# Performance work log

Hardware: AMD Instinct MI355X
Metric: run time of the kernel (lower is better)

The kernel has to match this reference:

```python
import jax, jax.numpy as jnp
import numpy as np

N_NODES = 100000
N_EDGES = 1600000
D_IN = 128
D_HID = 128
D_OUT = 40


def _linear_init(key, fan_in, fan_out):
    # torch nn.Linear default: U(-1/sqrt(fan_in), 1/sqrt(fan_in)) for W and b
    kw, kb = jax.random.split(key)
    bound = 1.0 / np.sqrt(fan_in)
    W = jax.random.uniform(kw, (fan_in, fan_out), jnp.float32, -bound, bound)
    b = jax.random.uniform(kb, (fan_out,), jnp.float32, -bound, bound)
    return W, b


def setup_inputs() -> dict:
    key = jax.random.key(0)
    ks = jax.random.split(key, 8)
    x = jax.random.normal(ks[0], (N_NODES, D_IN), jnp.float32)
    edges = jax.random.randint(ks[1], (2, N_EDGES), 0, N_NODES, jnp.int64)
    # layer 0: MLP(128 -> 128 -> 128)
    W1_0, b1_0 = _linear_init(ks[2], D_IN, D_HID)
    W2_0, b2_0 = _linear_init(ks[3], D_HID, D_HID)
    # layer 1: MLP(128 -> 128 -> 128)
    W1_1, b1_1 = _linear_init(ks[4], D_HID, D_HID)
    W2_1, b2_1 = _linear_init(ks[5], D_HID, D_HID)
    # layer 2: MLP(128 -> 128 -> 40)
    W1_2, b1_2 = _linear_init(ks[6], D_HID, D_HID)
    W2_2, b2_2 = _linear_init(ks[7], D_HID, D_OUT)
    eps = jnp.zeros(())  # GINConv train_eps=True initializes eps=0
    return {
        "x": x, "edges": edges,
        "W1_0": W1_0, "b1_0": b1_0, "W2_0": W2_0, "b2_0": b2_0, "eps_0": eps,
        "W1_1": W1_1, "b1_1": b1_1, "W2_1": W2_1, "b2_1": b2_1, "eps_1": eps,
        "W1_2": W1_2, "b1_2": b1_2, "W2_2": W2_2, "b2_2": b2_2, "eps_2": eps,
    }


def _gin_conv(x, src, dst, eps, W1, b1, W2, b2):
    # sum-aggregate neighbor features: out_i = MLP((1+eps)*x_i + sum_{j->i} x_j)
    aggr = jax.ops.segment_sum(x[src], dst, num_segments=x.shape[0])
    h = (1.0 + eps) * x + aggr
    h = jnp.maximum(h @ W1 + b1, 0.0)  # MLP layer 1 + ReLU
    return h @ W2 + b2                  # MLP layer 2


def reference(x, edges,
              W1_0, b1_0, W2_0, b2_0, eps_0,
              W1_1, b1_1, W2_1, b2_1, eps_1,
              W1_2, b1_2, W2_2, b2_2, eps_2):
    src, dst = edges[0], edges[1]
    # dropout is identity at inference (training=False)
    h = jax.nn.relu(_gin_conv(x, src, dst, eps_0, W1_0, b1_0, W2_0, b2_0))
    h = jax.nn.relu(_gin_conv(h, src, dst, eps_1, W1_1, b1_1, W2_1, b2_1))
    o = _gin_conv(h, src, dst, eps_2, W1_2, b1_2, W2_2, b2_2)
    return jax.nn.log_softmax(o, axis=1)
```

## Files before the change

### kernel.cpp

```cpp
#include <hip/hip_runtime.h>
#include <stdint.h>

typedef __attribute__((ext_vector_type(8))) short short8;
typedef __attribute__((ext_vector_type(4))) float float4v;

__device__ __forceinline__ float bf2f(unsigned short s) {
    union { unsigned int u; float f; } c; c.u = ((unsigned int)s) << 16; return c.f;
}
__device__ __forceinline__ unsigned short f2bf(float f) {
    union { float f; unsigned int u; } c; c.f = f;
    unsigned int x = c.u;
    unsigned int r = x + 0x7fffu + ((x >> 16) & 1u);
    return (unsigned short)(r >> 16);
}
__device__ __forceinline__ void unpack2(unsigned int u, float& lo, float& hi) {
    union { unsigned int uu; float ff; } a, b;
    a.uu = u << 16;
    b.uu = u & 0xffff0000u;
    lo = a.ff; hi = b.ff;
}

__global__ __launch_bounds__(256) void bs_count(const int* __restrict__ dst, int nE,
                                                int* __restrict__ bucketCnt) {
    __shared__ int c[512];
    int t = threadIdx.x;
    for (int i = t; i < 512; i += 256) c[i] = 0;
    __syncthreads();
    int base = blockIdx.x * 4096;
    for (int i = t; i < 4096; i += 256) {
        int e = base + i;
        if (e < nE) atomicAdd(&c[dst[e] >> 8], 1);
    }
    __syncthreads();
    for (int i = t; i < 512; i += 256)
        if (c[i]) atomicAdd(&bucketCnt[i], c[i]);
}

__global__ __launch_bounds__(512) void bs_scan(const int* __restrict__ bucketCnt,
                                               int* __restrict__ bucketBase,
                                               int* __restrict__ bucketCur,
                                               int* __restrict__ off, int M, int nE) {
    __shared__ int s[512];
    int t = threadIdx.x;
    int v = bucketCnt[t];
    s[t] = v;
    __syncthreads();
    for (int o = 1; o < 512; o <<= 1) {
        int x = (t >= o) ? s[t - o] : 0;
        __syncthreads();
        s[t] += x;
        __syncthreads();
    }
    bucketBase[t] = s[t] - v;
    bucketCur[t] = s[t] - v;
    if (t == 511) bucketBase[512] = s[511];
    if (t == 0) off[M] = nE;
}

__global__ __launch_bounds__(512) void bs_scatter(const int* __restrict__ src,
                                                  const int* __restrict__ dst, int nE,
                                                  int* __restrict__ bucketCur,
                                                  unsigned int* __restrict__ ebuf) {
    __shared__ int cnt[512];
    __shared__ int excl[512];
    __shared__ int chunk[512];
    __shared__ unsigned int buf[4096];
    __shared__ unsigned short bkt[4096];
    int t = threadIdx.x;
    cnt[t] = 0;
    __syncthreads();
    int base = blockIdx.x * 4096;
    int n = nE - base; if (n > 4096) n = 4096;
    unsigned int pk[8]; int bk[8]; int rk[8];
#pragma unroll
    for (int u = 0; u < 8; ++u) {
        int i = t + u * 512;
        if (i < n) {
            int e = base + i;
            int d = dst[e];
            int b = d >> 8;
            bk[u] = b;
            pk[u] = (unsigned int)src[e] | ((unsigned int)(d & 255) << 17);
            rk[u] = atomicAdd(&cnt[b], 1);
        } else bk[u] = -1;
    }
    __syncthreads();
    excl[t] = cnt[t];
    __syncthreads();
    for (int o = 1; o < 512; o <<= 1) {
        int x = (t >= o) ? excl[t - o] : 0;
        __syncthreads();
        excl[t] += x;
        __syncthreads();
    }
    int ex = excl[t] - cnt[t];
    __syncthreads();
    excl[t] = ex;
    if (cnt[t]) chunk[t] = atomicAdd(&bucketCur[t], cnt[t]);
    __syncthreads();
#pragma unroll
    for (int u = 0; u < 8; ++u) {
        if (bk[u] >= 0) {
            int lp = excl[bk[u]] + rk[u];
            buf[lp] = pk[u];
            bkt[lp] = (unsigned short)bk[u];
        }
    }
    __syncthreads();
    for (int i = t; i < n; i += 512) {
        int b = bkt[i];
        ebuf[chunk[b] + (i - excl[b])] = buf[i];
    }
}

__global__ __launch_bounds__(512) void bs_build(const unsigned int* __restrict__ ebuf,
                                                const int* __restrict__ bucketBase,
                                                int* __restrict__ off,
                                                int* __restrict__ esrc, int M) {
    __shared__ int cnt[256];
    __shared__ int excl[256];
    __shared__ int obuf[5120];
    int t = threadIdx.x, b = blockIdx.x;
    int base = bucketBase[b];
    int n = bucketBase[b + 1] - base;
    if (t < 256) cnt[t] = 0;
    __syncthreads();
    unsigned int pk[10]; int dl[10]; int rk[10];
#pragma unroll
    for (int u = 0; u < 10; ++u) {
        int i = t + u * 512;
        if (i < n) {
            unsigned int p = ebuf[base + i];
            pk[u] = p;
            int d = (p >> 17) & 255;
            dl[u] = d;
            rk[u] = atomicAdd(&cnt[d], 1);
        } else dl[u] = -1;
    }
    __syncthreads();
    if (t < 256) excl[t] = cnt[t];
    __syncthreads();
    for (int o = 1; o < 256; o <<= 1) {
        int x = (t < 256 && t >= o) ? excl[t - o] : 0;
        __syncthreads();
        if (t < 256) excl[t] += x;
        __syncthreads();
    }
    if (t < 256) {
        int ex = excl[t] - cnt[t];
        int node = b * 256 + t;
        if (node < M) off[node] = base + ex;
        excl[t] = ex;
    }
    __syncthreads();
#pragma unroll
    for (int u = 0; u < 10; ++u) {
        if (dl[u] >= 0) {
            int lp = excl[dl[u]] + rk[u];
            if (lp < 5120) obuf[lp] = (int)(pk[u] & 0x1FFFF);
        }
    }
    __syncthreads();
    for (int i = t; i < n; i += 512) esrc[base + i] = obuf[i];
}

struct WPack {
    const float* W[6];
    unsigned short* hi[6];
};

__global__ __launch_bounds__(256) void k_wprep_all(WPack p) {
    int b = blockIdx.x;
    int mat = b >> 6;
    int rel = b - mat * 64;
    int NPAD = (mat == 5) ? 48 : 128;
    int N = (mat == 5) ? 40 : 128;
    int idx = rel * 256 + threadIdx.x;
    if (idx >= NPAD * 128) return;
    int n = idx >> 7, k = idx & 127;
    float w = (n < N) ? p.W[mat][k * N + n] : 0.f;
    p.hi[mat][idx] = f2bf(w);
}

__global__ __launch_bounds__(256) void k_cast(const float4* __restrict__ in,
                                              uint2* __restrict__ out, int n4) {
    int i = blockIdx.x * 256 + threadIdx.x;
    if (i >= n4) return;
    float4 v = in[i];
    uint2 o;
    o.x = ((unsigned int)f2bf(v.y) << 16) | f2bf(v.x);
    o.y = ((unsigned int)f2bf(v.w) << 16) | f2bf(v.z);
    out[i] = o;
}

__global__ __launch_bounds__(256) void k_aggr(const uint2* __restrict__ Hin,
                                              const int* __restrict__ off,
                                              const int* __restrict__ esrc,
                                              const float* __restrict__ epsp,
                                              uint2* __restrict__ Ahi,
                                              uint2* __restrict__ Alo, int M) {
    int w = threadIdx.x >> 6, lane = threadIdx.x & 63;
    int li = lane & 31, half = lane >> 5;
    int node = blockIdx.x * 4 + w;
    if (node >= M) return;
    float ep = 1.0f + epsp[0];
    uint2 ow = Hin[node * 32 + li];
    float s0 = 0.f, s1 = 0.f, s2 = 0.f, s3 = 0.f;
    int i = off[node], e = off[node + 1];
    for (; i + 16 <= e; i += 16) {
        uint2 v[8];
#pragma unroll
        for (int j = 0; j < 8; ++j) v[j] = Hin[esrc[i + 2 * j + half] * 32 + li];
#pragma unroll
        for (int j = 0; j < 8; ++j) {
            float a, b, c, d;
            unpack2(v[j].x, a, b);
            unpack2(v[j].y, c, d);
            s0 += a; s1 += b; s2 += c; s3 += d;
        }
    }
    for (; i + 2 <= e; i += 2) {
        uint2 v = Hin[esrc[i + half] * 32 + li];
        float a, b, c, d;
        unpack2(v.x, a, b);
        unpack2(v.y, c, d);
        s0 += a; s1 += b; s2 += c; s3 += d;
    }
    if (i < e && half == 0) {
        uint2 v = Hin[esrc[i] * 32 + li];
        float a, b, c, d;
        unpack2(v.x, a, b);
        unpack2(v.y, c, d);
        s0 += a; s1 += b; s2 += c; s3 += d;
    }
    s0 += __shfl_xor(s0, 32);
    s1 += __shfl_xor(s1, 32);
    s2 += __shfl_xor(s2, 32);
    s3 += __shfl_xor(s3, 32);
    if (half == 0) {
        float o0, o1, o2, o3;
        unpack2(ow.x, o0, o1);
        unpack2(ow.y, o2, o3);
        float r0 = ep * o0 + s0, r1 = ep * o1 + s1;
        float r2 = ep * o2 + s2, r3 = ep * o3 + s3;
        unsigned short h0 = f2bf(r0), h1 = f2bf(r1), h2 = f2bf(r2), h3 = f2bf(r3);
        uint2 hi, lo;
        hi.x = ((unsigned int)h1 << 16) | h0;
        hi.y = ((unsigned int)h3 << 16) | h2;
        lo.x = ((unsigned int)f2bf(r1 - bf2f(h1)) << 16) | f2bf(r0 - bf2f(h0));
        lo.y = ((unsigned int)f2bf(r3 - bf2f(h3)) << 16) | f2bf(r2 - bf2f(h2));
        Ahi[node * 32 + li] = hi;
        Alo[node * 32 + li] = lo;
    }
}

template <int NT2, bool LOGITS>
__global__ __launch_bounds__(256, 3) void k_mlp(const unsigned short* __restrict__ AhiS,
                                                const unsigned short* __restrict__ AloS,
                                                const unsigned short* __restrict__ W1h,
                                                const float* __restrict__ B1,
                                                const unsigned short* __restrict__ W2h,
                                                const float* __restrict__ B2,
                                                unsigned short* __restrict__ HOut,
                                                float* __restrict__ LOut, int M) {
    __shared__ short wbuf[128 * 136];
    __shared__ short slab[4][16 * 136];
    int t = threadIdx.x, w = t >> 6, lane = t & 63;
    int lm = lane & 15, lg = lane >> 4;
    int rbase = blockIdx.x * 128;

    for (int i = t * 8; i < 128 * 128; i += 2048) {
        int n = i >> 7, k = i & 127;
        *(short8*)&wbuf[n * 136 + k] = *(const short8*)(W1h + i);
    }
    __syncthreads();

    short8 hh[2][4];
#pragma unroll
    for (int t2 = 0; t2 < 2; ++t2) {
        int r0 = rbase + t2 * 64 + w * 16;
        if (r0 < M) {
            const short* Ah = (const short*)AhiS + (r0 + lm) * 128 + lg * 8;
            const short* Al = (const short*)AloS + (r0 + lm) * 128 + lg * 8;
            short8 ah[4], al[4];
#pragma unroll
            for (int kb = 0; kb < 4; ++kb) {
                ah[kb] = *(const short8*)(Ah + kb * 32);
                al[kb] = *(const short8*)(Al + kb * 32);
            }
            float4v acc[8];
#pragma unroll
            for (int nt = 0; nt < 8; ++nt) acc[nt] = (float4v){0.f, 0.f, 0.f, 0.f};
#pragma unroll
            for (int nt = 0; nt < 8; ++nt) {
#pragma unroll
                for (int kb = 0; kb < 4; ++kb) {
                    short8 wh = *(const short8*)&wbuf[(nt * 16 + lm) * 136 + kb * 32 + lg * 8];
                    acc[nt] = __builtin_amdgcn_mfma_f32_16x16x32_bf16(ah[kb], wh, acc[nt], 0, 0, 0);
                    acc[nt] = __builtin_amdgcn_mfma_f32_16x16x32_bf16(al[kb], wh, acc[nt], 0, 0, 0);
                }
            }
#pragma unroll
            for (int nt = 0; nt < 8; ++nt) {
                float b = B1[nt * 16 + lm];
#pragma unroll
                for (int r = 0; r < 4; ++r) {
                    float v = acc[nt][r] + b;
                    v = v > 0.f ? v : 0.f;
                    slab[w][(lg * 4 + r) * 136 + nt * 16 + lm] = (short)f2bf(v);
                }
            }
#pragma unroll
            for (int kb = 0; kb < 4; ++kb)
                hh[t2][kb] = *(const short8*)&slab[w][lm * 136 + kb * 32 + lg * 8];
        }
    }

    __syncthreads();
    for (int i = t * 8; i < NT2 * 16 * 128; i += 2048) {
        int n = i >> 7, k = i & 127;
        *(short8*)&wbuf[n * 136 + k] = *(const short8*)(W2h + i);
    }
    __syncthreads();

#pragma unroll
    for (int t2 = 0; t2 < 2; ++t2) {
        int r0 = rbase + t2 * 64 + w * 16;
        if (r0 >= M) continue;
        float4v acc2[NT2];
#pragma unroll
        for (int nt = 0; nt < NT2; ++nt) acc2[nt] = (float4v){0.f, 0.f, 0.f, 0.f};
#pragma unroll
        for (int nt = 0; nt < NT2; ++nt) {
#pragma unroll
            for (int kb = 0; kb < 4; ++kb) {
                short8 wh = *(const short8*)&wbuf[(nt * 16 + lm) * 136 + kb * 32 + lg * 8];
                acc2[nt] = __builtin_amdgcn_mfma_f32_16x16x32_bf16(hh[t2][kb], wh, acc2[nt], 0, 0, 0);
            }
        }
        if (!LOGITS) {
#pragma unroll
            for (int nt = 0; nt < NT2; ++nt) {
                int col = nt * 16 + lm;
                float b = B2[col];
#pragma unroll
                for (int r = 0; r < 4; ++r) {
                    float v = acc2[nt][r] + b;
                    v = v > 0.f ? v : 0.f;
                    HOut[(r0 + lg * 4 + r) * 128 + col] = f2bf(v);
                }
            }
        } else {
            float vv[NT2][4];
#pragma unroll
            for (int nt = 0; nt < NT2; ++nt) {
                int col = nt * 16 + lm;
                bool valid = col < 40;
                float b = valid ? B2[col] : 0.f;
#pragma unroll
                for (int r = 0; r < 4; ++r)
                    vv[nt][r] = valid ? (acc2[nt][r] + b) : -1e30f;
            }
#pragma unroll
            for (int r = 0; r < 4; ++r) {
                float m = vv[0][r];
#pragma unroll
                for (int nt = 1; nt < NT2; ++nt) m = fmaxf(m, vv[nt][r]);
#pragma unroll
                for (int o = 8; o >= 1; o >>= 1) m = fmaxf(m, __shfl_xor(m, o, 64));
                float s = 0.f;
#pragma unroll
                for (int nt = 0; nt < NT2; ++nt)
                    s += (vv[nt][r] > -1e29f) ? expf(vv[nt][r] - m) : 0.f;
#pragma unroll
                for (int o = 8; o >= 1; o >>= 1) s += __shfl_xor(s, o, 64);
                float ls = m + logf(s);
                int row = r0 + lg * 4 + r;
#pragma unroll
                for (int nt = 0; nt < NT2; ++nt) {
                    int col = nt * 16 + lm;
                    if (col < 40) LOut[row * 40 + col] = vv[nt][r] - ls;
                }
            }
        }
    }
}

extern "C" void kernel_launch(void* const* d_in, const int* in_sizes, int n_in,
                              void* d_out, int out_size, void* d_ws, size_t ws_size,
                              hipStream_t stream) {
    const float* x    = (const float*)d_in[0];
    const int*   edges = (const int*)d_in[1];
    const float* eps0 = (const float*)d_in[6];
    const float* eps1 = (const float*)d_in[11];
    const float* eps2 = (const float*)d_in[16];
    const float* B1[3] = {(const float*)d_in[3], (const float*)d_in[8], (const float*)d_in[13]};
    const float* B2[3] = {(const float*)d_in[5], (const float*)d_in[10], (const float*)d_in[15]};

    int M  = in_sizes[0] / 128;
    int nE = in_sizes[1] / 2;
    const int* e_src = edges;
    const int* e_dst = edges + nE;

    char* ws = (char*)d_ws;
    size_t o = 0;
    auto alloc = [&](size_t bytes) {
        size_t p = o;
        o = (o + bytes + 511) & ~(size_t)511;
        return ws + p;
    };
    int* bucketCnt  = (int*)alloc(512 * 4);
    int* bucketBase = (int*)alloc(513 * 4);
    int* bucketCur  = (int*)alloc(512 * 4);
    int* off  = (int*)alloc((size_t)(M + 1) * 4);
    int* esrc = (int*)alloc((size_t)nE * 4);
    unsigned int* ebuf = (unsigned int*)alloc((size_t)nE * 4);

    WPack wp;
    wp.W[0] = (const float*)d_in[2];  wp.W[1] = (const float*)d_in[4];
    wp.W[2] = (const float*)d_in[7];  wp.W[3] = (const float*)d_in[9];
    wp.W[4] = (const float*)d_in[12]; wp.W[5] = (const float*)d_in[14];
    for (int m = 0; m < 6; ++m) {
        int npad = (m == 5) ? 48 : 128;
        wp.hi[m] = (unsigned short*)alloc((size_t)npad * 128 * 2);
    }
    unsigned short* xb  = (unsigned short*)alloc((size_t)M * 128 * 2);
    unsigned short* Ahi = (unsigned short*)alloc((size_t)M * 128 * 2);
    unsigned short* Alo = (unsigned short*)alloc((size_t)M * 128 * 2);
    unsigned short* Hb  = (unsigned short*)alloc((size_t)M * 128 * 2);
    (void)ws_size; (void)n_in; (void)out_size;

    hipMemsetAsync(bucketCnt, 0, 512 * 4, stream);
    int nChunk = (nE + 4095) / 4096;
    int nBk = (M + 255) / 256;
    bs_count<<<nChunk, 256, 0, stream>>>(e_dst, nE, bucketCnt);
    bs_scan<<<1, 512, 0, stream>>>(bucketCnt, bucketBase, bucketCur, off, M, nE);
    bs_scatter<<<nChunk, 512, 0, stream>>>(e_src, e_dst, nE, bucketCur, ebuf);
    bs_build<<<nBk, 512, 0, stream>>>(ebuf, bucketBase, off, esrc, M);
    k_wprep_all<<<344, 256, 0, stream>>>(wp);
    int n4 = M * 32;
    k_cast<<<(n4 + 255) / 256, 256, 0, stream>>>((const float4*)x, (uint2*)xb, n4);

    int gA = (M + 3) / 4;
    int gG = (M + 127) / 128;

    k_aggr<<<gA, 256, 0, stream>>>((const uint2*)xb, off, esrc, eps0,
                                   (uint2*)Ahi, (uint2*)Alo, M);
    k_mlp<8, false><<<gG, 256, 0, stream>>>(Ahi, Alo, wp.hi[0], B1[0],
                                            wp.hi[1], B2[0], Hb, nullptr, M);
    k_aggr<<<gA, 256, 0, stream>>>((const uint2*)Hb, off, esrc, eps1,
                                   (uint2*)Ahi, (uint2*)Alo, M);
    k_mlp<8, false><<<gG, 256, 0, stream>>>(Ahi, Alo, wp.hi[2], B1[1],
                                            wp.hi[3], B2[1], Hb, nullptr, M);
    k_aggr<<<gA, 256, 0, stream>>>((const uint2*)Hb, off, esrc, eps2,
                                   (uint2*)Ahi, (uint2*)Alo, M);
    k_mlp<3, true><<<gG, 256, 0, stream>>>(Ahi, Alo, wp.hi[4], B1[2],
                                           wp.hi[5], B2[2], nullptr,
                                           (float*)d_out, M);
}
```

Measured before the change: 466.5 us.

## Drop bf16 split-precision low part and map one node per half-wave in aggregation

Aggregation now writes only a single bf16 copy of the summed features, and the MLP kernel drops the second MFMA pass over the low-order residual. This halves the aggregate-buffer write and read traffic and the first-layer MFMA count, at the cost of lower numerical accuracy in the first GEMM input. The aggregation kernel also assigns one node to each 32-lane half-wave with an 8-wide clamped and masked gather loop, instead of splitting one node's edges across both halves. That removes the cross-half shuffle reduction and the scalar tail loops.

```diff
diff --git a/kernel.cpp b/kernel.cpp
--- a/kernel.cpp
+++ b/kernel.cpp
@@ -197,66 +197,47 @@
                                               const int* __restrict__ off,
                                               const int* __restrict__ esrc,
                                               const float* __restrict__ epsp,
-                                              uint2* __restrict__ Ahi,
-                                              uint2* __restrict__ Alo, int M) {
+                                              uint2* __restrict__ Ahi, int M) {
     int w = threadIdx.x >> 6, lane = threadIdx.x & 63;
     int li = lane & 31, half = lane >> 5;
-    int node = blockIdx.x * 4 + w;
+    int node = blockIdx.x * 8 + w * 2 + half;
     if (node >= M) return;
     float ep = 1.0f + epsp[0];
     uint2 ow = Hin[node * 32 + li];
     float s0 = 0.f, s1 = 0.f, s2 = 0.f, s3 = 0.f;
     int i = off[node], e = off[node + 1];
-    for (; i + 16 <= e; i += 16) {
+    int last = e - 1;
+    for (; i < e; i += 8) {
         uint2 v[8];
 #pragma unroll
-        for (int j = 0; j < 8; ++j) v[j] = Hin[esrc[i + 2 * j + half] * 32 + li];
-#pragma unroll
         for (int j = 0; j < 8; ++j) {
+            int idx = i + j;
+            int cl = idx < last ? idx : last;
+            v[j] = Hin[esrc[cl] * 32 + li];
+        }
+#pragma unroll
+        for (int j = 0; j < 8; ++j) {
+            unsigned int ux = (i + j < e) ? v[j].x : 0u;
+            unsigned int uy = (i + j < e) ? v[j].y : 0u;
             float a, b, c, d;
-            unpack2(v[j].x, a, b);
-            unpack2(v[j].y, c, d);
+            unpack2(ux, a, b);
+            unpack2(uy, c, d);
             s0 += a; s1 += b; s2 += c; s3 += d;
         }
     }
-    for (; i + 2 <= e; i += 2) {
-        uint2 v = Hin[esrc[i + half] * 32 + li];
-        float a, b, c, d;
-        unpack2(v.x, a, b);
-        unpack2(v.y, c, d);
-        s0 += a; s1 += b; s2 += c; s3 += d;
-    }
-    if (i < e && half == 0) {
-        uint2 v = Hin[esrc[i] * 32 + li];
-        float a, b, c, d;
-        unpack2(v.x, a, b);
-        unpack2(v.y, c, d);
-        s0 += a; s1 += b; s2 += c; s3 += d;
-    }
-    s0 += __shfl_xor(s0, 32);
-    s1 += __shfl_xor(s1, 32);
-    s2 += __shfl_xor(s2, 32);
-    s3 += __shfl_xor(s3, 32);
-    if (half == 0) {
-        float o0, o1, o2, o3;
-        unpack2(ow.x, o0, o1);
-        unpack2(ow.y, o2, o3);
-        float r0 = ep * o0 + s0, r1 = ep * o1 + s1;
-        float r2 = ep * o2 + s2, r3 = ep * o3 + s3;
-        unsigned short h0 = f2bf(r0), h1 = f2bf(r1), h2 = f2bf(r2), h3 = f2bf(r3);
-        uint2 hi, lo;
-        hi.x = ((unsigned int)h1 << 16) | h0;
-        hi.y = ((unsigned int)h3 << 16) | h2;
-        lo.x = ((unsigned int)f2bf(r1 - bf2f(h1)) << 16) | f2bf(r0 - bf2f(h0));
-        lo.y = ((unsigned int)f2bf(r3 - bf2f(h3)) << 16) | f2bf(r2 - bf2f(h2));
-        Ahi[node * 32 + li] = hi;
-        Alo[node * 32 + li] = lo;
-    }
+    float o0, o1, o2, o3;
+    unpack2(ow.x, o0, o1);
+    unpack2(ow.y, o2, o3);
+    float r0 = ep * o0 + s0, r1 = ep * o1 + s1;
+    float r2 = ep * o2 + s2, r3 = ep * o3 + s3;
+    uint2 hi;
+    hi.x = ((unsigned int)f2bf(r1) << 16) | f2bf(r0);
+    hi.y = ((unsigned int)f2bf(r3) << 16) | f2bf(r2);
+    Ahi[node * 32 + li] = hi;
 }
 
 template <int NT2, bool LOGITS>
 __global__ __launch_bounds__(256, 3) void k_mlp(const unsigned short* __restrict__ AhiS,
-                                                const unsigned short* __restrict__ AloS,
                                                 const unsigned short* __restrict__ W1h,
                                                 const float* __restrict__ B1,
                                                 const unsigned short* __restrict__ W2h,
@@ -281,13 +262,9 @@
         int r0 = rbase + t2 * 64 + w * 16;
         if (r0 < M) {
             const short* Ah = (const short*)AhiS + (r0 + lm) * 128 + lg * 8;
-            const short* Al = (const short*)AloS + (r0 + lm) * 128 + lg * 8;
-            short8 ah[4], al[4];
-#pragma unroll
-            for (int kb = 0; kb < 4; ++kb) {
-                ah[kb] = *(const short8*)(Ah + kb * 32);
-                al[kb] = *(const short8*)(Al + kb * 32);
-            }
+            short8 ah[4];
+#pragma unroll
+            for (int kb = 0; kb < 4; ++kb) ah[kb] = *(const short8*)(Ah + kb * 32);
             float4v acc[8];
 #pragma unroll
             for (int nt = 0; nt < 8; ++nt) acc[nt] = (float4v){0.f, 0.f, 0.f, 0.f};
@@ -297,7 +274,6 @@
                 for (int kb = 0; kb < 4; ++kb) {
                     short8 wh = *(const short8*)&wbuf[(nt * 16 + lm) * 136 + kb * 32 + lg * 8];
                     acc[nt] = __builtin_amdgcn_mfma_f32_16x16x32_bf16(ah[kb], wh, acc[nt], 0, 0, 0);
-                    acc[nt] = __builtin_amdgcn_mfma_f32_16x16x32_bf16(al[kb], wh, acc[nt], 0, 0, 0);
                 }
             }
 #pragma unroll
@@ -426,7 +402,6 @@
     }
     unsigned short* xb  = (unsigned short*)alloc((size_t)M * 128 * 2);
     unsigned short* Ahi = (unsigned short*)alloc((size_t)M * 128 * 2);
-    unsigned short* Alo = (unsigned short*)alloc((size_t)M * 128 * 2);
     unsigned short* Hb  = (unsigned short*)alloc((size_t)M * 128 * 2);
     (void)ws_size; (void)n_in; (void)out_size;
 
@@ -441,20 +416,17 @@
     int n4 = M * 32;
     k_cast<<<(n4 + 255) / 256, 256, 0, stream>>>((const float4*)x, (uint2*)xb, n4);
 
-    int gA = (M + 3) / 4;
+    int gA = (M + 7) / 8;
     int gG = (M + 127) / 128;
 
-    k_aggr<<<gA, 256, 0, stream>>>((const uint2*)xb, off, esrc, eps0,
-                                   (uint2*)Ahi, (uint2*)Alo, M);
-    k_mlp<8, false><<<gG, 256, 0, stream>>>(Ahi, Alo, wp.hi[0], B1[0],
+    k_aggr<<<gA, 256, 0, stream>>>((const uint2*)xb, off, esrc, eps0, (uint2*)Ahi, M);
+    k_mlp<8, false><<<gG, 256, 0, stream>>>(Ahi, wp.hi[0], B1[0],
                                             wp.hi[1], B2[0], Hb, nullptr, M);
-    k_aggr<<<gA, 256, 0, stream>>>((const uint2*)Hb, off, esrc, eps1,
-                                   (uint2*)Ahi, (uint2*)Alo, M);
-    k_mlp<8, false><<<gG, 256, 0, stream>>>(Ahi, Alo, wp.hi[2], B1[1],
+    k_aggr<<<gA, 256, 0, stream>>>((const uint2*)Hb, off, esrc, eps1, (uint2*)Ahi, M);
+    k_mlp<8, false><<<gG, 256, 0, stream>>>(Ahi, wp.hi[2], B1[1],
                                             wp.hi[3], B2[1], Hb, nullptr, M);
-    k_aggr<<<gA, 256, 0, stream>>>((const uint2*)Hb, off, esrc, eps2,
-                                   (uint2*)Ahi, (uint2*)Alo, M);
-    k_mlp<3, true><<<gG, 256, 0, stream>>>(Ahi, Alo, wp.hi[4], B1[2],
+    k_aggr<<<gA, 256, 0, stream>>>((const uint2*)Hb, off, esrc, eps2, (uint2*)Ahi, M);
+    k_mlp<3, true><<<gG, 256, 0, stream>>>(Ahi, wp.hi[4], B1[2],
                                            wp.hi[5], B2[2], nullptr,
                                            (float*)d_out, M);
 }
```

Result: faster. 410.0 us (-12.1%).
